# Optimization experiments

Hardware: AMD Instinct MI355X
Metric: run time of the kernel (lower is better)

The kernel has to match this reference:

```python
import jax, jax.numpy as jnp
import numpy as np
import math

EPS = 1.0
DELT = 1e-05
CLIP = 1.0
N_LOCS = 1000000
EMB_DIM = 64
N_EDGES = 4000000


def setup_inputs() -> dict:
    key = jax.random.key(0)
    k1, k2, k3 = jax.random.split(key, 3)
    loc_emb = jax.random.normal(k1, (N_LOCS, EMB_DIM), dtype=jnp.float32)
    noise = jax.random.normal(k2, (N_EDGES, EMB_DIM), dtype=jnp.float32)
    edge_locs = jax.random.randint(k3, (N_EDGES,), 0, N_LOCS, dtype=jnp.int32)
    return {"loc_emb": loc_emb, "noise": noise, "edge_locs": edge_locs}


def reference(loc_emb, noise, edge_locs):
    n_locs = loc_emb.shape[0]
    # sigma = clip * sqrt(2 * ln(1.25/delta)) / eps  (Gaussian mechanism)
    sigma = CLIP * math.sqrt(2.0 * math.log(1.25 / DELT)) / EPS
    # edge_cnt[loc] = number of edges touching loc (Counter over real+fake)
    edge_cnt = jax.ops.segment_sum(
        jnp.ones_like(edge_locs, dtype=loc_emb.dtype), edge_locs,
        num_segments=n_locs)
    # per-edge scaled noise: sigma * n / edge_cnt[loc]; every referenced loc has cnt>=1
    inv_cnt = (sigma / edge_cnt[edge_locs])[:, None]  # [E, 1]
    loc_noise = jax.ops.segment_sum(noise * inv_cnt, edge_locs,
                                    num_segments=n_locs)  # [n_locs, d]
    return loc_emb + loc_noise
```

## Files before the change

kernel.cpp:

```cpp
#include <hip/hip_runtime.h>
#include <math.h>

#define EMB 64

typedef float f32x4 __attribute__((ext_vector_type(4)));
typedef int   i32x4 __attribute__((ext_vector_type(4)));


__global__ void count_rank_k(const int* __restrict__ el, int* __restrict__ cnt,
                             int* __restrict__ rank, int n4, int n) {
    int i = blockIdx.x * blockDim.x + threadIdx.x;
    if (i >= n4) return;
    int base = i * 4;
    i32x4 e = *(reinterpret_cast<const i32x4*>(el) + i);
    i32x4 r;
    r.x = atomicAdd(cnt + e.x, 1);
    r.y = (base + 1 < n) ? atomicAdd(cnt + e.y, 1) : 0;
    r.z = (base + 2 < n) ? atomicAdd(cnt + e.z, 1) : 0;
    r.w = (base + 3 < n) ? atomicAdd(cnt + e.w, 1) : 0;
    *(reinterpret_cast<i32x4*>(rank) + i) = r;
}

__global__ void block_sum_k(const int* __restrict__ cnt, int* __restrict__ part, int n) {
    __shared__ int s[256];
    int i = blockIdx.x * 256 + threadIdx.x;
    s[threadIdx.x] = (i < n) ? cnt[i] : 0;
    __syncthreads();
    for (int off = 128; off > 0; off >>= 1) {
        if (threadIdx.x < off) s[threadIdx.x] += s[threadIdx.x + off];
        __syncthreads();
    }
    if (threadIdx.x == 0) part[blockIdx.x] = s[0];
}

__global__ void scan_part_k(int* __restrict__ part, int nb) {
    __shared__ int s[4096];
    for (int i = threadIdx.x; i < 4096; i += 1024) s[i] = (i < nb) ? part[i] : 0;
    __syncthreads();
    for (int off = 1; off < 4096; off <<= 1) {
        int vals[4];
        #pragma unroll
        for (int j = 0; j < 4; ++j) {
            int i = threadIdx.x + j * 1024;
            vals[j] = (i >= off) ? s[i - off] : 0;
        }
        __syncthreads();
        #pragma unroll
        for (int j = 0; j < 4; ++j) {
            int i = threadIdx.x + j * 1024;
            s[i] += vals[j];
        }
        __syncthreads();
    }
    for (int i = threadIdx.x; i < nb; i += 1024) part[i] = (i == 0) ? 0 : s[i - 1];
}

__global__ void scan_meta_k(const int* __restrict__ cnt, const int* __restrict__ part,
                            int2* __restrict__ meta, int n) {
    __shared__ int s[256];
    int i = blockIdx.x * 256 + threadIdx.x;
    int v = (i < n) ? cnt[i] : 0;
    s[threadIdx.x] = v;
    __syncthreads();
    for (int off = 1; off < 256; off <<= 1) {
        int t = (threadIdx.x >= (unsigned)off) ? s[threadIdx.x - off] : 0;
        __syncthreads();
        s[threadIdx.x] += t;
        __syncthreads();
    }
    if (i < n) {
        int2 m;
        m.x = s[threadIdx.x] - v + part[blockIdx.x];
        m.y = v;
        meta[i] = m;
    }
}

__global__ void fill_csr_k(const int* __restrict__ el, const int* __restrict__ rank,
                           const int2* __restrict__ meta, int* __restrict__ csr,
                           int n4, int n) {
    int i = blockIdx.x * blockDim.x + threadIdx.x;
    if (i >= n4) return;
    int base = i * 4;
    i32x4 e = *(reinterpret_cast<const i32x4*>(el) + i);
    i32x4 r = *(reinterpret_cast<const i32x4*>(rank) + i);
    csr[meta[e.x].x + r.x] = base;
    if (base + 1 < n) csr[meta[e.y].x + r.y] = base + 1;
    if (base + 2 < n) csr[meta[e.z].x + r.z] = base + 2;
    if (base + 3 < n) csr[meta[e.w].x + r.w] = base + 3;
}


__device__ __forceinline__ f32x4 ld_row(const float* noise, int e, int q) {
    return *(reinterpret_cast<const f32x4*>(noise + ((long long)e << 6)) + q);
}

__global__ void gather_k(const float* __restrict__ loc_emb, const float* __restrict__ noise,
                         const int2* __restrict__ meta, const int* __restrict__ csr,
                         float* __restrict__ out, float sigma, int n_locs) {
    int gid = blockIdx.x * blockDim.x + threadIdx.x;
    int loc = gid >> 4;
    if (loc >= n_locs) return;
    int q = gid & 15;
    int2 m = meta[loc];
    int st = m.x, c = m.y;
    f32x4 acc = (f32x4)(0.f);
    for (int i = 0; i < c; i += 8) {
        int r = c - i;
        int b0 = st + i;
        int e[8];
        #pragma unroll
        for (int j = 0; j < 8; ++j)
            e[j] = csr[b0 + (j < r ? j : r - 1)];
        f32x4 v[8];
        #pragma unroll
        for (int j = 0; j < 8; ++j)
            v[j] = ld_row(noise, e[j], q);
        #pragma unroll
        for (int j = 0; j < 8; ++j)
            if (j < r) acc += v[j];
    }
    float s = (c > 0) ? sigma / (float)c : 0.f;
    const f32x4* bp = reinterpret_cast<const f32x4*>(loc_emb + ((long long)loc << 6)) + q;
    f32x4 b = __builtin_nontemporal_load(bp);
    f32x4 o = b + s * acc;
    f32x4* op = reinterpret_cast<f32x4*>(out + ((long long)loc << 6)) + q;
    __builtin_nontemporal_store(o, op);
}

extern "C" void kernel_launch(void* const* d_in, const int* in_sizes, int n_in,
                              void* d_out, int out_size, void* d_ws, size_t ws_size,
                              hipStream_t stream) {
    const float* loc_emb = (const float*)d_in[0];
    const float* noise   = (const float*)d_in[1];
    const int*   el      = (const int*)d_in[2];
    float* out = (float*)d_out;

    int n_locs  = in_sizes[0] / EMB;
    int n_edges = in_sizes[2];

    char* w = (char*)d_ws;
    int*  cnt  = (int*)w;                 w += (size_t)n_locs * sizeof(int);
    int*  part = (int*)w;                 w += 4096 * sizeof(int);
    int2* meta = (int2*)w;                w += (size_t)n_locs * sizeof(int2);
    int*  rank = (int*)w;                 w += (size_t)n_edges * sizeof(int);
    int*  csr  = (int*)w;

    int nb = (n_locs + 255) / 256;
    int n4 = (n_edges + 3) / 4;

    (void)hipMemsetAsync(cnt, 0, (size_t)n_locs * sizeof(int), stream);

    count_rank_k<<<(n4 + 255) / 256, 256, 0, stream>>>(el, cnt, rank, n4, n_edges);
    block_sum_k<<<nb, 256, 0, stream>>>(cnt, part, n_locs);
    scan_part_k<<<1, 1024, 0, stream>>>(part, nb);
    scan_meta_k<<<nb, 256, 0, stream>>>(cnt, part, meta, n_locs);
    fill_csr_k<<<(n4 + 255) / 256, 256, 0, stream>>>(el, rank, meta, csr, n4, n_edges);

    double sigma = 1.0 * sqrt(2.0 * log(1.25 / 1e-5)) / 1.0;
    long long total = (long long)n_locs * 16;
    int blocks = (int)((total + 255) / 256);
    gather_k<<<blocks, 256, 0, stream>>>(loc_emb, noise, meta, csr, out,
                                         (float)sigma, n_locs);
}
```

Before: 556.2 us.

## Use scalar per-edge count/fill kernels and nontemporal predicated noise gathers

Reverts the count and CSR-fill kernels from four edges per thread to one edge per thread, which gives more threads and fewer serialized atomics per thread. In the gather kernel, noise rows are now read with nontemporal loads, and the CSR index and noise loads are predicated instead of clamped, so tail iterations issue no redundant loads. The loc_emb load is also hoisted ahead of the accumulation loop so it overlaps with the gathers. Costs are larger grids for the preprocessing kernels and the risk that nontemporal loads bypass useful caching.

New measurement: 552.6 us. About the same (-0.6%).

```diff
diff --git a/kernel.cpp b/kernel.cpp
--- a/kernel.cpp
+++ b/kernel.cpp
@@ -4,21 +4,12 @@
 #define EMB 64
 
 typedef float f32x4 __attribute__((ext_vector_type(4)));
-typedef int   i32x4 __attribute__((ext_vector_type(4)));
 
 
 __global__ void count_rank_k(const int* __restrict__ el, int* __restrict__ cnt,
-                             int* __restrict__ rank, int n4, int n) {
+                             int* __restrict__ rank, int n) {
     int i = blockIdx.x * blockDim.x + threadIdx.x;
-    if (i >= n4) return;
-    int base = i * 4;
-    i32x4 e = *(reinterpret_cast<const i32x4*>(el) + i);
-    i32x4 r;
-    r.x = atomicAdd(cnt + e.x, 1);
-    r.y = (base + 1 < n) ? atomicAdd(cnt + e.y, 1) : 0;
-    r.z = (base + 2 < n) ? atomicAdd(cnt + e.z, 1) : 0;
-    r.w = (base + 3 < n) ? atomicAdd(cnt + e.w, 1) : 0;
-    *(reinterpret_cast<i32x4*>(rank) + i) = r;
+    if (i < n) rank[i] = atomicAdd(cnt + el[i], 1);
 }
 
 __global__ void block_sum_k(const int* __restrict__ cnt, int* __restrict__ part, int n) {
@@ -77,22 +68,15 @@
 }
 
 __global__ void fill_csr_k(const int* __restrict__ el, const int* __restrict__ rank,
-                           const int2* __restrict__ meta, int* __restrict__ csr,
-                           int n4, int n) {
+                           const int2* __restrict__ meta, int* __restrict__ csr, int n) {
     int i = blockIdx.x * blockDim.x + threadIdx.x;
-    if (i >= n4) return;
-    int base = i * 4;
-    i32x4 e = *(reinterpret_cast<const i32x4*>(el) + i);
-    i32x4 r = *(reinterpret_cast<const i32x4*>(rank) + i);
-    csr[meta[e.x].x + r.x] = base;
-    if (base + 1 < n) csr[meta[e.y].x + r.y] = base + 1;
-    if (base + 2 < n) csr[meta[e.z].x + r.z] = base + 2;
-    if (base + 3 < n) csr[meta[e.w].x + r.w] = base + 3;
+    if (i < n) csr[meta[el[i]].x + rank[i]] = i;
 }
 
 
-__device__ __forceinline__ f32x4 ld_row(const float* noise, int e, int q) {
-    return *(reinterpret_cast<const f32x4*>(noise + ((long long)e << 6)) + q);
+__device__ __forceinline__ f32x4 ld_row_nt(const float* noise, int e, int q) {
+    const f32x4* p = reinterpret_cast<const f32x4*>(noise + ((long long)e << 6)) + q;
+    return __builtin_nontemporal_load(p);
 }
 
 __global__ void gather_k(const float* __restrict__ loc_emb, const float* __restrict__ noise,
@@ -104,25 +88,25 @@
     int q = gid & 15;
     int2 m = meta[loc];
     int st = m.x, c = m.y;
+    const f32x4* bp = reinterpret_cast<const f32x4*>(loc_emb + ((long long)loc << 6)) + q;
+    f32x4 b = __builtin_nontemporal_load(bp);
     f32x4 acc = (f32x4)(0.f);
     for (int i = 0; i < c; i += 8) {
         int r = c - i;
         int b0 = st + i;
         int e[8];
-        #pragma unroll
-        for (int j = 0; j < 8; ++j)
-            e[j] = csr[b0 + (j < r ? j : r - 1)];
         f32x4 v[8];
         #pragma unroll
         for (int j = 0; j < 8; ++j)
-            v[j] = ld_row(noise, e[j], q);
+            if (j < r) e[j] = csr[b0 + j];
+        #pragma unroll
+        for (int j = 0; j < 8; ++j)
+            if (j < r) v[j] = ld_row_nt(noise, e[j], q);
         #pragma unroll
         for (int j = 0; j < 8; ++j)
             if (j < r) acc += v[j];
     }
     float s = (c > 0) ? sigma / (float)c : 0.f;
-    const f32x4* bp = reinterpret_cast<const f32x4*>(loc_emb + ((long long)loc << 6)) + q;
-    f32x4 b = __builtin_nontemporal_load(bp);
     f32x4 o = b + s * acc;
     f32x4* op = reinterpret_cast<f32x4*>(out + ((long long)loc << 6)) + q;
     __builtin_nontemporal_store(o, op);
@@ -147,15 +131,14 @@
     int*  csr  = (int*)w;
 
     int nb = (n_locs + 255) / 256;
-    int n4 = (n_edges + 3) / 4;
 
     (void)hipMemsetAsync(cnt, 0, (size_t)n_locs * sizeof(int), stream);
 
-    count_rank_k<<<(n4 + 255) / 256, 256, 0, stream>>>(el, cnt, rank, n4, n_edges);
+    count_rank_k<<<(n_edges + 255) / 256, 256, 0, stream>>>(el, cnt, rank, n_edges);
     block_sum_k<<<nb, 256, 0, stream>>>(cnt, part, n_locs);
     scan_part_k<<<1, 1024, 0, stream>>>(part, nb);
     scan_meta_k<<<nb, 256, 0, stream>>>(cnt, part, meta, n_locs);
-    fill_csr_k<<<(n4 + 255) / 256, 256, 0, stream>>>(el, rank, meta, csr, n4, n_edges);
+    fill_csr_k<<<(n_edges + 255) / 256, 256, 0, stream>>>(el, rank, meta, csr, n_edges);
 
     double sigma = 1.0 * sqrt(2.0 * log(1.25 / 1e-5)) / 1.0;
     long long total = (long long)n_locs * 16;
```
